# Kernel optimization log

Measured on AMD Instinct MI355X. Metric: run time of the kernel, lower is better.

The kernel has to match this reference:

```python
import jax, jax.numpy as jnp
import numpy as np

B, C, H, W = 2, 256, 64, 64  # C = in_channels; x has 2*C channels
DQ = C // 16


def setup_inputs() -> dict:
    key = jax.random.key(0)
    ks = jax.random.split(key, 10)
    s = 0.05
    return {
        "x": jax.random.normal(ks[0], (B, 2 * C, H, W), dtype=jnp.float32),
        "Wq": jax.random.normal(ks[1], (DQ, C), dtype=jnp.float32) * s,
        "bq": jax.random.normal(ks[2], (DQ,), dtype=jnp.float32) * s,
        "Wk": jax.random.normal(ks[3], (DQ, C), dtype=jnp.float32) * s,
        "bk": jax.random.normal(ks[4], (DQ,), dtype=jnp.float32) * s,
        "Wv": jax.random.normal(ks[5], (C, C), dtype=jnp.float32) * s,
        "bv": jax.random.normal(ks[6], (C,), dtype=jnp.float32) * s,
        "Wpt": jax.random.normal(ks[7], (C, 2 * C), dtype=jnp.float32) * s,
        "bpt": jax.random.normal(ks[8], (C,), dtype=jnp.float32) * s,
        "gamma": jnp.full((1,), 0.5, dtype=jnp.float32),  # original inits to 0; nonzero for a non-trivial output
    }


def _conv1x1(x, Wt, b):
    # 1x1 conv == per-pixel linear map over channels
    return jnp.einsum("bchw,dc->bdhw", x, Wt) + b[None, :, None, None]


def reference(x, Wq, bq, Wk, bk, Wv, bv, Wpt, bpt, gamma):
    n = x.shape[1] // 2
    x1, x2 = x[:, :n], x[:, n:]
    b, c, h, w = x1.shape
    hw = h * w

    def qkv(xi):
        q = _conv1x1(xi, Wq, bq).reshape(b, DQ, hw)   # [B,dq,HW]
        k = _conv1x1(xi, Wk, bk).reshape(b, DQ, hw)   # [B,dq,HW]
        v = _conv1x1(xi, Wv, bv).reshape(b, c, hw)    # [B,C,HW]
        return q, k, v

    q1, k1, v1 = qkv(x1)
    q2, k2, v2 = qkv(x2)

    # attn[b,i,j] = softmax_j( q[:,i] . k[:,j] )  (no scaling, as in original)
    attn1 = jax.nn.softmax(jnp.einsum("bdi,bdj->bij", q1, k1), axis=-1)  # [B,HW,HW]
    attn2 = jax.nn.softmax(jnp.einsum("bdi,bdj->bij", q2, k2), axis=-1)

    def apply_attn(v, attn):
        # out[b,c,i] = sum_j v[b,c,j] * attn[b,i,j]
        return jnp.einsum("bcj,bij->bci", v, attn).reshape(b, c, h, w)

    out11 = apply_attn(v1, attn1)
    out12 = apply_attn(v2, attn1)
    out21 = apply_attn(v1, attn2)
    out22 = apply_attn(v2, attn2)

    o1 = _conv1x1(jnp.concatenate([out11, out12], axis=1), Wpt, bpt)  # [B,C,H,W]
    o2 = _conv1x1(jnp.concatenate([out21, out22], axis=1), Wpt, bpt)

    out = gamma * jnp.concatenate([o1, o2], axis=1) + x
    return out
```

## Files before the change

kernel.cpp:

```cpp
#include <hip/hip_runtime.h>
#include <hip/hip_bf16.h>


#define HW 4096
#define CC 256
#define DQ 16

typedef __hip_bfloat16 bf16;
struct alignas(8) bh4 { bf16 x, y, z, w; };
typedef __bf16 bf16x8 __attribute__((ext_vector_type(8)));
typedef float  f32x4  __attribute__((ext_vector_type(4)));

static __device__ __forceinline__ float b2f(bf16 v) { return __bfloat162float(v); }

static __device__ __forceinline__ void load_lds16(const void* g, void* l) {
    __builtin_amdgcn_global_load_lds(
        (const __attribute__((address_space(1))) unsigned int*)g,
        (__attribute__((address_space(3))) unsigned int*)l, 16, 0, 0);
}

static __device__ __forceinline__ bf16x8 ones8() {
    union { unsigned int u[4]; bf16x8 v; } t;
    t.u[0] = t.u[1] = t.u[2] = t.u[3] = 0x3F803F80u;
    return t.v;
}

struct ConvArgs { const void* src[9]; float* dst[9]; int n[9]; };
__global__ void convert_weights(ConvArgs a, const unsigned short* __restrict__ probe) {
    int seg = blockIdx.y;
    int i = blockIdx.x * 256 + threadIdx.x;
    bool isb = probe[0] != 0;
    if (i < a.n[seg])
        a.dst[seg][i] = isb ? b2f(((const bf16*)a.src[seg])[i])
                            : ((const float*)a.src[seg])[i];
}

__global__ void w_to_bf16(const float* __restrict__ Wqf, const float* __restrict__ Wkf,
                          bf16* __restrict__ Wqb, bf16* __restrict__ Wkb) {
    int i = blockIdx.x * 256 + threadIdx.x;
    const float* s = blockIdx.y ? Wkf : Wqf;
    bf16* d = blockIdx.y ? Wkb : Wqb;
    d[i] = __float2bfloat16(s[i]);
}

__global__ void convert_x_t(const void* __restrict__ xsrc, bf16* __restrict__ Xt,
                            const unsigned short* __restrict__ probe) {
    __shared__ float T[64][65];
    int t = threadIdx.x;
    int j0 = blockIdx.x * 64, e0 = blockIdx.y * 64, b = blockIdx.z;
    bool isb = probe[0] != 0;
    int j_l = t & 63, er0 = (t >> 6) * 16;
#pragma unroll
    for (int r = 0; r < 16; ++r) {
        size_t src = ((size_t)(b * 512 + e0 + er0 + r)) * HW + j0 + j_l;
        T[er0 + r][j_l] = isb ? b2f(((const bf16*)xsrc)[src]) : ((const float*)xsrc)[src];
    }
    __syncthreads();
    int e_w = t & 63, jr0 = (t >> 6) * 16;
#pragma unroll
    for (int r = 0; r < 16; ++r)
        Xt[((size_t)b * HW + j0 + jr0 + r) * 512 + e0 + e_w] = __float2bfloat16(T[e_w][jr0 + r]);
}

__global__ void build_mc(const float* __restrict__ Wv, const float* __restrict__ bv,
                         const float* __restrict__ Wpt, const float* __restrict__ bpt,
                         bf16* __restrict__ McB, float* __restrict__ btot) {
    int blk = blockIdx.x, tid = threadIdx.x;
    if (blk < 512) {
        int d = blk >> 1;
        int c = ((blk & 1) << 8) + tid;
        int half = c >> 8, cm = c & 255;
        float acc = 0.f;
        for (int e = 0; e < 256; ++e)
            acc = fmaf(Wpt[d * 512 + half * 256 + e], Wv[e * 256 + cm], acc);
        McB[d * 512 + c] = __float2bfloat16(acc);
    } else {
        int d = tid;
        float acc = bpt[d];
        for (int e = 0; e < 256; ++e)
            acc = fmaf(Wpt[d * 512 + e] + Wpt[d * 512 + 256 + e], bv[e], acc);
        btot[d] = acc;
    }
}

__global__ void __launch_bounds__(256)
build_qk_mfma(const bf16* __restrict__ Xt,
              const bf16* __restrict__ Wqb, const float* __restrict__ bqf,
              const bf16* __restrict__ Wkb, const float* __restrict__ bkf,
              bf16* __restrict__ Qb, bf16* __restrict__ Kb) {
    int tid = threadIdx.x;
    int lane = tid & 63, wave = tid >> 6;
    int ln = lane & 15, q = lane >> 4;
    int bh = blockIdx.y;
    int b = bh >> 1, h = bh & 1;
    int j0 = blockIdx.x * 64 + wave * 16;

    bf16x8 aQ[8], aK[8];
#pragma unroll
    for (int kk = 0; kk < 8; ++kk) {
        aQ[kk] = *(const bf16x8*)&Wqb[ln * 256 + kk * 32 + q * 8];
        aK[kk] = *(const bf16x8*)&Wkb[ln * 256 + kk * 32 + q * 8];
    }
    const bf16* Xrow = Xt + ((size_t)b * HW + j0 + ln) * 512 + h * 256;
    f32x4 dQ = {0.f, 0.f, 0.f, 0.f}, dK = {0.f, 0.f, 0.f, 0.f};
#pragma unroll
    for (int kk = 0; kk < 8; ++kk) {
        bf16x8 bx = *(const bf16x8*)&Xrow[kk * 32 + q * 8];
        dQ = __builtin_amdgcn_mfma_f32_16x16x32_bf16(aQ[kk], bx, dQ, 0, 0, 0);
        dK = __builtin_amdgcn_mfma_f32_16x16x32_bf16(aK[kk], bx, dK, 0, 0, 0);
    }
    size_t rowoff = ((size_t)bh * HW + j0 + ln) * 32;
    bh4 oq, ok;
    oq.x = __float2bfloat16(dQ[0] + bqf[q * 4 + 0]);
    oq.y = __float2bfloat16(dQ[1] + bqf[q * 4 + 1]);
    oq.z = __float2bfloat16(dQ[2] + bqf[q * 4 + 2]);
    oq.w = __float2bfloat16(dQ[3] + bqf[q * 4 + 3]);
    ok.x = __float2bfloat16(dK[0] + bkf[q * 4 + 0]);
    ok.y = __float2bfloat16(dK[1] + bkf[q * 4 + 1]);
    ok.z = __float2bfloat16(dK[2] + bkf[q * 4 + 2]);
    ok.w = __float2bfloat16(dK[3] + bkf[q * 4 + 3]);
    bh4 z; z.x = z.y = z.z = z.w = __float2bfloat16(0.f);
    *(bh4*)&Qb[rowoff + q * 4] = oq;
    *(bh4*)&Qb[rowoff + 16 + q * 4] = z;
    *(bh4*)&Kb[rowoff + q * 4] = ok;
    *(bh4*)&Kb[rowoff + 16 + q * 4] = z;
}

__global__ void __launch_bounds__(256, 2)
build_u_mfma(const bf16* __restrict__ McB, const bf16* __restrict__ Xt,
             bf16* __restrict__ Ub) {
    __shared__ __align__(16) bf16 sA[64 * 64];
    __shared__ __align__(16) bf16 sB[128 * 64];
    int tid = threadIdx.x;
    int lane = tid & 63, wave = tid >> 6;
    int ln = lane & 15, q = lane >> 4;
    int wm = (wave >> 1) * 32, wn = (wave & 1) * 64;
    int j0 = blockIdx.x * 128, c0 = blockIdx.y * 64, b = blockIdx.z;
    const bf16* Xb = Xt + (size_t)b * HW * 512;
    f32x4 acc[2][4];
#pragma unroll
    for (int mi = 0; mi < 2; ++mi)
#pragma unroll
        for (int ni = 0; ni < 4; ++ni)
#pragma unroll
            for (int r = 0; r < 4; ++r) acc[mi][ni][r] = 0.f;

    for (int e0 = 0; e0 < 512; e0 += 64) {
        __syncthreads();
#pragma unroll
        for (int r = 0; r < 2; ++r) {
            int s = r * 256 + tid;
            int row = s >> 3, jc = s & 7, jg = jc ^ (row & 7);
            load_lds16(McB + (size_t)(c0 + row) * 512 + e0 + jg * 8, sA + s * 8);
        }
#pragma unroll
        for (int r = 0; r < 4; ++r) {
            int s = r * 256 + tid;
            int row = s >> 3, jc = s & 7, jg = jc ^ (row & 7);
            load_lds16(Xb + (size_t)(j0 + row) * 512 + e0 + jg * 8, sB + s * 8);
        }
        __syncthreads();
#pragma unroll
        for (int kh = 0; kh < 2; ++kh) {
            bf16x8 af[2], bfv[4];
#pragma unroll
            for (int mi = 0; mi < 2; ++mi) {
                int row = wm + mi * 16 + ln;
                int jc = (kh * 4 + q) ^ (row & 7);
                af[mi] = *(const bf16x8*)&sA[row * 64 + jc * 8];
            }
#pragma unroll
            for (int ni = 0; ni < 4; ++ni) {
                int row = wn + ni * 16 + ln;
                int jc = (kh * 4 + q) ^ (row & 7);
                bfv[ni] = *(const bf16x8*)&sB[row * 64 + jc * 8];
            }
#pragma unroll
            for (int mi = 0; mi < 2; ++mi)
#pragma unroll
                for (int ni = 0; ni < 4; ++ni)
                    acc[mi][ni] = __builtin_amdgcn_mfma_f32_16x16x32_bf16(
                        af[mi], bfv[ni], acc[mi][ni], 0, 0, 0);
        }
    }
#pragma unroll
    for (int mi = 0; mi < 2; ++mi)
#pragma unroll
        for (int r = 0; r < 4; ++r) {
            int c = c0 + wm + mi * 16 + q * 4 + r;
#pragma unroll
            for (int ni = 0; ni < 4; ++ni) {
                int j = j0 + wn + ni * 16 + ln;
                Ub[((size_t)(b * CC + c)) * HW + j] = __float2bfloat16(acc[mi][ni][r]);
            }
        }
}

__global__ void __launch_bounds__(256, 2)
flash_attn(const bf16* __restrict__ Ub, const bf16* __restrict__ Qb,
           const bf16* __restrict__ Kb, const float* __restrict__ btot,
           const void* __restrict__ xorig, const float* __restrict__ gamf,
           void* __restrict__ outv, const unsigned short* __restrict__ probe) {
    __shared__ __align__(16) bf16 sU[128 * 64];
    __shared__ __align__(16) bf16 sE[64 * 64];
    int tid  = threadIdx.x;
    int lane = tid & 63, wave = tid >> 6;
    int ln = lane & 15, q = lane >> 4;
    int wm = (wave & 1) * 64, wn = (wave >> 1) * 32;
    int i0 = blockIdx.x * 64, c0 = blockIdx.y * 128;
    int bh = blockIdx.z;
    int b = bh >> 1, h = bh & 1;
    const bf16* Ubb = Ub + (size_t)b * CC * HW + (size_t)c0 * HW;
    const bf16* Kbh = Kb + (size_t)bh * HW * 32;
    const bf16x8 ONE = ones8();

    bf16x8 bq = *(const bf16x8*)&Qb[((size_t)bh * HW + i0 + wave * 16 + ln) * 32 + q * 8];

    f32x4 acc[4][2], accS[2];
#pragma unroll
    for (int ni = 0; ni < 2; ++ni) {
#pragma unroll
        for (int r = 0; r < 4; ++r) accS[ni][r] = 0.f;
#pragma unroll
        for (int mi = 0; mi < 4; ++mi)
#pragma unroll
            for (int r = 0; r < 4; ++r) acc[mi][ni][r] = 0.f;
    }

    int i_loc = wave * 16 + ln;
    int wchunk0 = (q >> 1);
    int woff = (q & 1) * 4;

    for (int j0 = 0; j0 < HW; j0 += 64) {
        __syncthreads();
#pragma unroll
        for (int r = 0; r < 4; ++r) {
            int s = r * 256 + tid;
            int row = s >> 3, jc = s & 7, jg = jc ^ (row & 7);
            load_lds16(Ubb + (size_t)row * HW + j0 + jg * 8, sU + s * 8);
        }
#pragma unroll
        for (int js = 0; js < 4; ++js) {
            bf16x8 ak = *(const bf16x8*)&Kbh[(size_t)(j0 + js * 16 + ln) * 32 + q * 8];
            f32x4 d = {0.f, 0.f, 0.f, 0.f};
            d = __builtin_amdgcn_mfma_f32_16x16x32_bf16(ak, bq, d, 0, 0, 0);
            bh4 o;
            o.x = __float2bfloat16(__expf(d[0]));
            o.y = __float2bfloat16(__expf(d[1]));
            o.z = __float2bfloat16(__expf(d[2]));
            o.w = __float2bfloat16(__expf(d[3]));
            int chunk = (js * 2 + wchunk0) ^ (i_loc & 7);
            *(bh4*)&sE[i_loc * 64 + chunk * 8 + woff] = o;
        }
        __syncthreads();
#pragma unroll
        for (int kh = 0; kh < 2; ++kh) {
            bf16x8 af[4], bfv[2];
#pragma unroll
            for (int mi = 0; mi < 4; ++mi) {
                int row = wm + mi * 16 + ln;
                int jc = (kh * 4 + q) ^ (row & 7);
                af[mi] = *(const bf16x8*)&sU[row * 64 + jc * 8];
            }
#pragma unroll
            for (int ni = 0; ni < 2; ++ni) {
                int row = wn + ni * 16 + ln;
                int jc = (kh * 4 + q) ^ (row & 7);
                bfv[ni] = *(const bf16x8*)&sE[row * 64 + jc * 8];
            }
#pragma unroll
            for (int ni = 0; ni < 2; ++ni) {
                accS[ni] = __builtin_amdgcn_mfma_f32_16x16x32_bf16(
                    ONE, bfv[ni], accS[ni], 0, 0, 0);
#pragma unroll
                for (int mi = 0; mi < 4; ++mi)
                    acc[mi][ni] = __builtin_amdgcn_mfma_f32_16x16x32_bf16(
                        af[mi], bfv[ni], acc[mi][ni], 0, 0, 0);
            }
        }
    }

    bool isb = probe[0] != 0;
    float g = gamf[0];
    float lv[2];
#pragma unroll
    for (int ni = 0; ni < 2; ++ni)
        lv[ni] = 1.f / accS[ni][0];
#pragma unroll
    for (int mi = 0; mi < 4; ++mi)
#pragma unroll
        for (int r = 0; r < 4; ++r) {
            int c = c0 + wm + mi * 16 + q * 4 + r;
            float bt = btot[c];
            size_t rowbase = ((size_t)(b * 512 + h * 256 + c)) * HW + i0 + wn;
#pragma unroll
            for (int ni = 0; ni < 2; ++ni) {
                size_t idx = rowbase + ni * 16 + ln;
                float xres = isb ? b2f(((const bf16*)xorig)[idx]) : ((const float*)xorig)[idx];
                float o = fmaf(g, fmaf(acc[mi][ni][r], lv[ni], bt), xres);
                if (isb) ((bf16*)outv)[idx] = __float2bfloat16(o);
                else     ((float*)outv)[idx] = o;
            }
        }
}

extern "C" void kernel_launch(void* const* d_in, const int* in_sizes, int n_in,
                              void* d_out, int out_size, void* d_ws, size_t ws_size,
                              hipStream_t stream) {
    const unsigned short* probe = (const unsigned short*)d_in[9];

    char* ws = (char*)d_ws;
    size_t off = 0;
    auto alloc = [&](size_t bytes) { size_t r = off; off = (off + bytes + 255) & ~(size_t)255; return r; };
    const int wsz[9] = {DQ * 256, DQ, DQ * 256, DQ, 256 * 256, 256, 256 * 512, 256, 1};
    float* wf[9];
    for (int t = 0; t < 9; ++t) wf[t] = (float*)(ws + alloc((size_t)wsz[t] * 4));
    bf16*  Xt   = (bf16*)(ws + alloc((size_t)2 * HW * 512 * 2));
    bf16*  McB  = (bf16*)(ws + alloc(256 * 512 * 2));
    float* btot = (float*)(ws + alloc(256 * 4));
    bf16*  Wqb  = (bf16*)(ws + alloc(DQ * 256 * 2));
    bf16*  Wkb  = (bf16*)(ws + alloc(DQ * 256 * 2));
    bf16*  Qb   = (bf16*)(ws + alloc((size_t)4 * HW * 32 * 2));
    bf16*  Kb   = (bf16*)(ws + alloc((size_t)4 * HW * 32 * 2));
    bf16*  Ub   = (bf16*)(ws + alloc((size_t)2 * CC * HW * 2));

    ConvArgs ca;
    for (int t = 0; t < 9; ++t) { ca.src[t] = d_in[t + 1]; ca.dst[t] = wf[t]; ca.n[t] = wsz[t]; }
    convert_weights<<<dim3(512, 9), 256, 0, stream>>>(ca, probe);
    w_to_bf16<<<dim3(16, 2), 256, 0, stream>>>(wf[0], wf[2], Wqb, Wkb);
    convert_x_t<<<dim3(64, 8, 2), 256, 0, stream>>>(d_in[0], Xt, probe);

    build_mc<<<513, 256, 0, stream>>>(wf[4], wf[5], wf[6], wf[7], McB, btot);
    build_qk_mfma<<<dim3(64, 4), 256, 0, stream>>>(Xt, Wqb, wf[1], Wkb, wf[3], Qb, Kb);
    build_u_mfma<<<dim3(32, 4, 2), 256, 0, stream>>>(McB, Xt, Ub);

    flash_attn<<<dim3(64, 2, 4), 256, 0, stream>>>(Ub, Qb, Kb, btot, d_in[0], wf[8], d_out, probe);
}
```

Baseline: 207.7 us.

## Shrink flash_attn channel tile to 64 and give each wave private query rows

The attention kernel now tiles 64 channels per block instead of 128, which doubles the grid to 1024 blocks. Each wave owns its own 16 query rows and keeps a per-wave exp tile in LDS. Launch bounds are raised to 4 blocks per CU to lift occupancy. The trade-off is that each block now recomputes the QK^T exponentials for half as many channels, so the exp work doubles overall, and MFMA reuse of the E fragments per LDS load drops.

```diff
diff --git a/kernel.cpp b/kernel.cpp
--- a/kernel.cpp
+++ b/kernel.cpp
@@ -196,45 +196,42 @@
         }
 }
 
-__global__ void __launch_bounds__(256, 2)
+__global__ void __launch_bounds__(256, 4)
 flash_attn(const bf16* __restrict__ Ub, const bf16* __restrict__ Qb,
            const bf16* __restrict__ Kb, const float* __restrict__ btot,
            const void* __restrict__ xorig, const float* __restrict__ gamf,
            void* __restrict__ outv, const unsigned short* __restrict__ probe) {
-    __shared__ __align__(16) bf16 sU[128 * 64];
-    __shared__ __align__(16) bf16 sE[64 * 64];
+    __shared__ __align__(16) bf16 sU[64 * 64];
+    __shared__ __align__(16) bf16 sE[4][16 * 64];
     int tid  = threadIdx.x;
     int lane = tid & 63, wave = tid >> 6;
     int ln = lane & 15, q = lane >> 4;
-    int wm = (wave & 1) * 64, wn = (wave >> 1) * 32;
-    int i0 = blockIdx.x * 64, c0 = blockIdx.y * 128;
+    int i0 = blockIdx.x * 64, c0 = blockIdx.y * 64;
     int bh = blockIdx.z;
     int b = bh >> 1, h = bh & 1;
     const bf16* Ubb = Ub + (size_t)b * CC * HW + (size_t)c0 * HW;
     const bf16* Kbh = Kb + (size_t)bh * HW * 32;
     const bf16x8 ONE = ones8();
+    bf16* sEw = &sE[wave][0];
 
     bf16x8 bq = *(const bf16x8*)&Qb[((size_t)bh * HW + i0 + wave * 16 + ln) * 32 + q * 8];
 
-    f32x4 acc[4][2], accS[2];
-#pragma unroll
-    for (int ni = 0; ni < 2; ++ni) {
-#pragma unroll
-        for (int r = 0; r < 4; ++r) accS[ni][r] = 0.f;
-#pragma unroll
-        for (int mi = 0; mi < 4; ++mi)
-#pragma unroll
-            for (int r = 0; r < 4; ++r) acc[mi][ni][r] = 0.f;
-    }
-
-    int i_loc = wave * 16 + ln;
-    int wchunk0 = (q >> 1);
+    f32x4 acc[4], accS;
+#pragma unroll
+    for (int r = 0; r < 4; ++r) accS[r] = 0.f;
+#pragma unroll
+    for (int mi = 0; mi < 4; ++mi)
+#pragma unroll
+        for (int r = 0; r < 4; ++r) acc[mi][r] = 0.f;
+
+    int wchunk0 = q >> 1;
     int woff = (q & 1) * 4;
 
-    for (int j0 = 0; j0 < HW; j0 += 64) {
+    for (int t = 0; t < 64; ++t) {
+        int j0 = t * 64;
         __syncthreads();
 #pragma unroll
-        for (int r = 0; r < 4; ++r) {
+        for (int r = 0; r < 2; ++r) {
             int s = r * 256 + tid;
             int row = s >> 3, jc = s & 7, jg = jc ^ (row & 7);
             load_lds16(Ubb + (size_t)row * HW + j0 + jg * 8, sU + s * 8);
@@ -249,58 +246,39 @@
             o.y = __float2bfloat16(__expf(d[1]));
             o.z = __float2bfloat16(__expf(d[2]));
             o.w = __float2bfloat16(__expf(d[3]));
-            int chunk = (js * 2 + wchunk0) ^ (i_loc & 7);
-            *(bh4*)&sE[i_loc * 64 + chunk * 8 + woff] = o;
+            int chunk = (js * 2 + wchunk0) ^ (ln & 7);
+            *(bh4*)&sEw[ln * 64 + chunk * 8 + woff] = o;
         }
         __syncthreads();
 #pragma unroll
         for (int kh = 0; kh < 2; ++kh) {
-            bf16x8 af[4], bfv[2];
+            int jcE = (kh * 4 + q) ^ (ln & 7);
+            bf16x8 bfv = *(const bf16x8*)&sEw[ln * 64 + jcE * 8];
+            accS = __builtin_amdgcn_mfma_f32_16x16x32_bf16(ONE, bfv, accS, 0, 0, 0);
 #pragma unroll
             for (int mi = 0; mi < 4; ++mi) {
-                int row = wm + mi * 16 + ln;
+                int row = mi * 16 + ln;
                 int jc = (kh * 4 + q) ^ (row & 7);
-                af[mi] = *(const bf16x8*)&sU[row * 64 + jc * 8];
-            }
-#pragma unroll
-            for (int ni = 0; ni < 2; ++ni) {
-                int row = wn + ni * 16 + ln;
-                int jc = (kh * 4 + q) ^ (row & 7);
-                bfv[ni] = *(const bf16x8*)&sE[row * 64 + jc * 8];
-            }
-#pragma unroll
-            for (int ni = 0; ni < 2; ++ni) {
-                accS[ni] = __builtin_amdgcn_mfma_f32_16x16x32_bf16(
-                    ONE, bfv[ni], accS[ni], 0, 0, 0);
-#pragma unroll
-                for (int mi = 0; mi < 4; ++mi)
-                    acc[mi][ni] = __builtin_amdgcn_mfma_f32_16x16x32_bf16(
-                        af[mi], bfv[ni], acc[mi][ni], 0, 0, 0);
+                bf16x8 af = *(const bf16x8*)&sU[row * 64 + jc * 8];
+                acc[mi] = __builtin_amdgcn_mfma_f32_16x16x32_bf16(af, bfv, acc[mi], 0, 0, 0);
             }
         }
     }
 
     bool isb = probe[0] != 0;
     float g = gamf[0];
-    float lv[2];
-#pragma unroll
-    for (int ni = 0; ni < 2; ++ni)
-        lv[ni] = 1.f / accS[ni][0];
+    float lv = 1.f / accS[0];
+    int i = i0 + wave * 16 + ln;
 #pragma unroll
     for (int mi = 0; mi < 4; ++mi)
 #pragma unroll
         for (int r = 0; r < 4; ++r) {
-            int c = c0 + wm + mi * 16 + q * 4 + r;
-            float bt = btot[c];
-            size_t rowbase = ((size_t)(b * 512 + h * 256 + c)) * HW + i0 + wn;
-#pragma unroll
-            for (int ni = 0; ni < 2; ++ni) {
-                size_t idx = rowbase + ni * 16 + ln;
-                float xres = isb ? b2f(((const bf16*)xorig)[idx]) : ((const float*)xorig)[idx];
-                float o = fmaf(g, fmaf(acc[mi][ni][r], lv[ni], bt), xres);
-                if (isb) ((bf16*)outv)[idx] = __float2bfloat16(o);
-                else     ((float*)outv)[idx] = o;
-            }
+            int c = c0 + mi * 16 + q * 4 + r;
+            size_t idx = ((size_t)(b * 512 + h * 256 + c)) * HW + i;
+            float xres = isb ? b2f(((const bf16*)xorig)[idx]) : ((const float*)xorig)[idx];
+            float o = fmaf(g, fmaf(acc[mi][r], lv, btot[c]), xres);
+            if (isb) ((bf16*)outv)[idx] = __float2bfloat16(o);
+            else     ((float*)outv)[idx] = o;
         }
 }
 
@@ -334,5 +312,5 @@
     build_qk_mfma<<<dim3(64, 4), 256, 0, stream>>>(Xt, Wqb, wf[1], Wkb, wf[3], Qb, Kb);
     build_u_mfma<<<dim3(32, 4, 2), 256, 0, stream>>>(McB, Xt, Ub);
 
-    flash_attn<<<dim3(64, 2, 4), 256, 0, stream>>>(Ub, Qb, Kb, btot, d_in[0], wf[8], d_out, probe);
-}
+    flash_attn<<<dim3(64, 4, 4), 256, 0, stream>>>(Ub, Qb, Kb, btot, d_in[0], wf[8], d_out, probe);
+}
```

Measured after the change: 215.7 us. 3.9% more time.
